# Optimization experiments

Measured on AMD Instinct MI355X. Metric: run time of the kernel, lower is better.

The kernel has to match this reference:

```python
import jax, jax.numpy as jnp
import numpy as np

N_HEAD = 16
MASKED_BIAS = -10000.0


def setup_inputs() -> dict:
    key = jax.random.key(0)
    k1, k2, k3 = jax.random.split(key, 3)
    B, T, E = 2, 2048, 1024
    return {
        "stacked": jax.random.normal(k1, (B, T, E), dtype=jnp.float32),
        "w_attn": jax.random.normal(k2, (E, 3 * E), dtype=jnp.float32) * 0.02,
        "b_attn": jnp.zeros((3 * E,), dtype=jnp.float32),
        "w_proj": jax.random.normal(k3, (E, E), dtype=jnp.float32) * 0.02,
        "b_proj": jnp.zeros((E,), dtype=jnp.float32),
    }


def reference(stacked, w_attn, b_attn, w_proj, b_proj):
    B, T, E = stacked.shape
    nh = N_HEAD
    dh = E // nh
    # Conv1D (GPT-2): x @ W + b
    qkv = stacked @ w_attn + b_attn            # (B, T, 3E)
    q, k, v = jnp.split(qkv, 3, axis=-1)
    q = q.reshape(B, T, nh, dh).transpose(0, 2, 1, 3)  # (B, nh, T, dh)
    k = k.reshape(B, T, nh, dh).transpose(0, 2, 1, 3)
    v = v.reshape(B, T, nh, dh).transpose(0, 2, 1, 3)
    # scores = Q @ K^T / sqrt(dh)
    w = jnp.einsum("bhtd,bhsd->bhts", q, k) / jnp.sqrt(jnp.float32(dh))
    causal = jnp.tril(jnp.ones((T, T), dtype=bool))
    w = jnp.where(causal, w, jnp.float32(MASKED_BIAS))
    w = jax.nn.softmax(w, axis=-1)
    out = jnp.einsum("bhts,bhsd->bhtd", w, v)  # (B, nh, T, dh)
    out = out.transpose(0, 2, 1, 3).reshape(B, T, E)
    attn_z = out @ w_proj + b_proj
    return attn_z
```

## Files before the change

kernel.cpp:

```cpp
#include <hip/hip_runtime.h>
#include <hip/hip_bf16.h>

#define B_ 2
#define T_ 2048
#define E_ 1024
#define NH 16
#define M_ (B_*T_)
#define N3E 3072

typedef __attribute__((ext_vector_type(8))) short short8;
typedef __attribute__((ext_vector_type(4))) float f32x4;

__device__ __forceinline__ unsigned short f2bf(float f) {
  unsigned u = __builtin_bit_cast(unsigned, f);
  unsigned r = 0x7FFFu + ((u >> 16) & 1u);
  return (unsigned short)((u + r) >> 16);
}

__device__ __forceinline__ float bf2f(unsigned short s) {
  return __builtin_bit_cast(float, ((unsigned)s) << 16);
}

__device__ __forceinline__ unsigned cvtpk(float a, float b) {
  unsigned r;
  asm("v_cvt_pk_bf16_f32 %0, %1, %2" : "=v"(r) : "v"(a), "v"(b));
  return r;
}

__device__ __forceinline__ float exp2fast(float x) {
  float r;
  asm("v_exp_f32 %0, %1" : "=v"(r) : "v"(x));
  return r;
}

__device__ __forceinline__ void gload16(const void* g, void* l) {
  __builtin_amdgcn_global_load_lds(
      (const __attribute__((address_space(1))) unsigned int*)g,
      (__attribute__((address_space(3))) unsigned int*)l, 16, 0, 0);
}

__device__ __forceinline__ f32x4 mfma16(short8 a, short8 b, f32x4 c) {
  return __builtin_amdgcn_mfma_f32_16x16x32_bf16(a, b, c, 0, 0, 0);
}

__global__ __launch_bounds__(256) void prep_kernel(
    const float* __restrict__ stacked, const float* __restrict__ w_attn,
    const float* __restrict__ w_proj, unsigned short* __restrict__ Abf,
    unsigned short* __restrict__ WaT, unsigned short* __restrict__ WpT) {
  __shared__ float tile[32][33];
  const int bx = blockIdx.x;
  const int tid = threadIdx.x;
  if (bx < 2048) {
    int i = bx * 256 + tid;
    const float4* p = (const float4*)stacked + (size_t)i * 2;
    float4 a = p[0], b = p[1];
    short8 o;
    o[0] = (short)f2bf(a.x); o[1] = (short)f2bf(a.y);
    o[2] = (short)f2bf(a.z); o[3] = (short)f2bf(a.w);
    o[4] = (short)f2bf(b.x); o[5] = (short)f2bf(b.y);
    o[6] = (short)f2bf(b.z); o[7] = (short)f2bf(b.w);
    *(short8*)(Abf + (size_t)i * 8) = o;
    return;
  }
  const float* in;
  unsigned short* out;
  int R, C, c0, r0;
  if (bx < 5120) {
    int b = bx - 2048;
    in = w_attn; out = WaT; R = E_; C = N3E;
    c0 = (b % 96) * 32; r0 = (b / 96) * 32;
  } else {
    int b = bx - 5120;
    in = w_proj; out = WpT; R = E_; C = E_;
    c0 = (b % 32) * 32; r0 = (b / 32) * 32;
  }
  int tx = tid & 31, ty = tid >> 5;
#pragma unroll
  for (int i = 0; i < 4; i++) {
    int r = ty + i * 8;
    tile[r][tx] = in[(size_t)(r0 + r) * C + c0 + tx];
  }
  __syncthreads();
#pragma unroll
  for (int i = 0; i < 4; i++) {
    int r = ty + i * 8;
    out[(size_t)(c0 + r) * R + r0 + tx] = f2bf(tile[tx][r]);
  }
}

__global__ __launch_bounds__(512, 1) void gemm256(
    const unsigned short* __restrict__ A, const unsigned short* __restrict__ Bt,
    const float* __restrict__ bias, unsigned short* __restrict__ qkvout,
    unsigned short* __restrict__ Vt, int M, int N, int K) {
  __shared__ __attribute__((aligned(16))) unsigned short Asm[2][256 * 64];
  __shared__ __attribute__((aligned(16))) unsigned short Bsm[2][192 * 64];
  const int tid = threadIdx.x;
  const int lane = tid & 63, wid = tid >> 6;
  const int wr = wid >> 2, wcn = wid & 3;
  const int li = lane & 15, g = lane >> 4;
  const int sw = li & 7;

  const int ntx = N / 192;
  const int nwg = (M >> 8) * ntx;
  const int cpx = nwg >> 3;
  const int logical = (blockIdx.x & 7) * cpx + (blockIdx.x >> 3);
  const int bm = (logical / ntx) << 8;
  const int bn = (logical % ntx) * 192;

  f32x4 acc[8][3] = {};

#pragma unroll
  for (int p = 0; p < 4; p++) {
    int idx = tid + p * 512;
    int r = idx >> 3, ch = idx & 7;
    gload16(A + (size_t)(bm + r) * K + ((ch ^ (r & 7)) << 3),
            (char*)&Asm[0][0] + idx * 16);
  }
#pragma unroll
  for (int p = 0; p < 3; p++) {
    int idx = tid + p * 512;
    int r = idx >> 3, ch = idx & 7;
    gload16(Bt + (size_t)(bn + r) * K + ((ch ^ (r & 7)) << 3),
            (char*)&Bsm[0][0] + idx * 16);
  }
  asm volatile("s_waitcnt vmcnt(0)" ::: "memory");
  __syncthreads();

  const int NT = K >> 6;
  for (int t = 0; t < NT; t++) {
    const int buf = t & 1;
    const unsigned short* As = &Asm[buf][0];
    const unsigned short* Bs = &Bsm[buf][0];
    const int kn = (t + 1) << 6;
    const bool pre = (t + 1 < NT);
    short8 a[4][2];
#pragma unroll
    for (int ph = 0; ph < 6; ph++) {
      const int mh = ph / 3, nf3 = ph % 3;
      if (nf3 == 0) {
#pragma unroll
        for (int mf = 0; mf < 4; mf++) {
          const int R = wr * 128 + (mh * 4 + mf) * 16 + li;
          a[mf][0] = *(const short8*)&As[R * 64 + ((g ^ sw) << 3)];
          a[mf][1] = *(const short8*)&As[R * 64 + (((4 + g) ^ sw) << 3)];
        }
      }
      const int S = wcn * 48 + nf3 * 16 + li;
      short8 b0 = *(const short8*)&Bs[S * 64 + ((g ^ sw) << 3)];
      short8 b1 = *(const short8*)&Bs[S * 64 + (((4 + g) ^ sw) << 3)];
      if (pre && ph == 0) {
#pragma unroll
        for (int p = 0; p < 4; p++) {
          int idx = tid + p * 512;
          int r = idx >> 3, ch = idx & 7;
          gload16(A + (size_t)(bm + r) * K + kn + ((ch ^ (r & 7)) << 3),
                  (char*)&Asm[buf ^ 1][0] + idx * 16);
        }
      }
      if (pre && ph == 1) {
#pragma unroll
        for (int p = 0; p < 3; p++) {
          int idx = tid + p * 512;
          int r = idx >> 3, ch = idx & 7;
          gload16(Bt + (size_t)(bn + r) * K + kn + ((ch ^ (r & 7)) << 3),
                  (char*)&Bsm[buf ^ 1][0] + idx * 16);
        }
      }
      __builtin_amdgcn_sched_barrier(0);
      __builtin_amdgcn_s_setprio(1);
#pragma unroll
      for (int mf = 0; mf < 4; mf++) {
        f32x4 c = acc[mh * 4 + mf][nf3];
        c = mfma16(a[mf][0], b0, c);
        c = mfma16(a[mf][1], b1, c);
        acc[mh * 4 + mf][nf3] = c;
      }
      __builtin_amdgcn_s_setprio(0);
      __builtin_amdgcn_sched_barrier(0);
    }
    asm volatile("s_waitcnt vmcnt(0)" ::: "memory");
    __syncthreads();
  }

#pragma unroll
  for (int nf = 0; nf < 3; nf++) {
    int col = bn + wcn * 48 + nf * 16 + li;
    float bs = bias[col];
    if (col < 2 * E_) {
#pragma unroll
      for (int mf = 0; mf < 8; mf++) {
        int row0 = bm + wr * 128 + mf * 16 + g * 4;
#pragma unroll
        for (int r = 0; r < 4; r++)
          qkvout[(size_t)(row0 + r) * N + col] = f2bf(acc[mf][nf][r] + bs);
      }
    } else {
      const int c = col - 2 * E_;
#pragma unroll
      for (int mf = 0; mf < 8; mf++) {
        int row0 = bm + wr * 128 + mf * 16 + g * 4;
        int bq = row0 >> 11, s0 = row0 & 2047;
        uint2 o;
        o.x = cvtpk(acc[mf][nf][0] + bs, acc[mf][nf][1] + bs);
        o.y = cvtpk(acc[mf][nf][2] + bs, acc[mf][nf][3] + bs);
        *(uint2*)&Vt[(size_t)(bq * E_ + c) * T_ + s0] = o;
      }
    }
  }
}

template <int OUTF32>
__global__ __launch_bounds__(256) void gemm_bt(
    const unsigned short* __restrict__ A, const unsigned short* __restrict__ Bt,
    const float* __restrict__ bias, void* __restrict__ outp,
    int M, int N, int K) {
  __shared__ __attribute__((aligned(16))) unsigned short Asm[2][128 * 32];
  __shared__ __attribute__((aligned(16))) unsigned short Bsm[2][128 * 32];
  const int tid = threadIdx.x;
  const int lane = tid & 63;
  const int wid = tid >> 6;
  const int wr = wid >> 1, wc = wid & 1;
  const int li = lane & 15, g = lane >> 4;

  const int ntx = N >> 7;
  const int nwg = (M >> 7) * ntx;
  const int cpx = nwg >> 3;
  const int logical = (blockIdx.x & 7) * cpx + (blockIdx.x >> 3);
  const int bm = (logical / ntx) << 7;
  const int bn = (logical % ntx) << 7;

  f32x4 acc[4][4] = {};

  const int srow = tid >> 2;
  const int scol = (tid & 3) * 8;
  const unsigned short* Ag = A + (size_t)(bm + srow) * K + scol;
  const unsigned short* Bg = Bt + (size_t)(bn + srow) * K + scol;
  const int ldsoff = tid * 16;

  gload16(Ag, (char*)&Asm[0][0] + ldsoff);
  gload16(Ag + (size_t)64 * K, (char*)&Asm[0][0] + ldsoff + 4096);
  gload16(Bg, (char*)&Bsm[0][0] + ldsoff);
  gload16(Bg + (size_t)64 * K, (char*)&Bsm[0][0] + ldsoff + 4096);
  asm volatile("s_waitcnt vmcnt(0)" ::: "memory");
  __syncthreads();

  int cur = 0;
  for (int k0 = 0; k0 < K; k0 += 32) {
    const bool pre = (k0 + 32 < K);
    if (pre) {
      const int k1 = k0 + 32;
      gload16(Ag + k1, (char*)&Asm[cur ^ 1][0] + ldsoff);
      gload16(Ag + (size_t)64 * K + k1,
              (char*)&Asm[cur ^ 1][0] + ldsoff + 4096);
      gload16(Bg + k1, (char*)&Bsm[cur ^ 1][0] + ldsoff);
      gload16(Bg + (size_t)64 * K + k1,
              (char*)&Bsm[cur ^ 1][0] + ldsoff + 4096);
    }
    short8 af[4], bf[4];
#pragma unroll
    for (int i = 0; i < 4; i++)
      af[i] = *(const short8*)&Asm[cur][(wr * 64 + i * 16 + li) * 32 + g * 8];
#pragma unroll
    for (int j = 0; j < 4; j++)
      bf[j] = *(const short8*)&Bsm[cur][(wc * 64 + j * 16 + li) * 32 + g * 8];
    __builtin_amdgcn_s_setprio(1);
#pragma unroll
    for (int i = 0; i < 4; i++)
#pragma unroll
      for (int j = 0; j < 4; j++)
        acc[i][j] = __builtin_amdgcn_mfma_f32_16x16x32_bf16(af[i], bf[j],
                                                            acc[i][j], 0, 0, 0);
    __builtin_amdgcn_s_setprio(0);
    if (pre) asm volatile("s_waitcnt vmcnt(0)" ::: "memory");
    __syncthreads();
    cur ^= 1;
  }

#pragma unroll
  for (int j = 0; j < 4; j++) {
    int col = bn + wc * 64 + j * 16 + li;
    float bs = bias[col];
#pragma unroll
    for (int i = 0; i < 4; i++) {
      int row0 = bm + wr * 64 + i * 16 + g * 4;
#pragma unroll
      for (int r = 0; r < 4; r++) {
        float v = acc[i][j][r] + bs;
        if (OUTF32)
          ((float*)outp)[(size_t)(row0 + r) * N + col] = v;
        else
          ((unsigned short*)outp)[(size_t)(row0 + r) * N + col] = f2bf(v);
      }
    }
  }
}

__device__ __forceinline__ void attn_tile(
    const unsigned short* Ksm, const unsigned short* Vts,
    unsigned short (*PsmW)[64], short8 qf0, short8 qf1,
    float& m2, float& l2, f32x4* O, int qrel, bool diag, int li, int g) {
  f32x4 S[4];
  __builtin_amdgcn_s_setprio(1);
#pragma unroll
  for (int ct = 0; ct < 4; ct++) {
    int r = ct * 16 + li;
    int sw = r & 7;
    short8 k0f = *(const short8*)&Ksm[r * 64 + ((g ^ sw) << 3)];
    short8 k1f = *(const short8*)&Ksm[r * 64 + (((g + 4) ^ sw) << 3)];
    f32x4 z = {0.f, 0.f, 0.f, 0.f};
    z = mfma16(k0f, qf0, z);
    z = mfma16(k1f, qf1, z);
    S[ct] = z;
  }
  __builtin_amdgcn_s_setprio(0);

  if (diag) {
#pragma unroll
    for (int ct = 0; ct < 4; ct++)
#pragma unroll
      for (int r = 0; r < 4; r++)
        if (ct * 16 + g * 4 + r > qrel) S[ct][r] = -30000.f;
  }

  float tmax = S[0][0];
#pragma unroll
  for (int ct = 0; ct < 4; ct++)
#pragma unroll
    for (int r = 0; r < 4; r++) tmax = fmaxf(tmax, S[ct][r]);
  tmax = fmaxf(tmax, __shfl_xor(tmax, 16));
  tmax = fmaxf(tmax, __shfl_xor(tmax, 32));

  if (__any(tmax > m2 + 11.5f)) {
    float mn = fmaxf(m2, tmax);
    float cs = exp2fast(m2 - mn);
    l2 *= cs;
#pragma unroll
    for (int c2 = 0; c2 < 4; c2++)
#pragma unroll
      for (int r = 0; r < 4; r++) O[c2][r] *= cs;
    m2 = mn;
  }

  float rsum = 0.f;
#pragma unroll
  for (int ct = 0; ct < 4; ct++) {
    float p0 = exp2fast(S[ct][0] - m2);
    float p1 = exp2fast(S[ct][1] - m2);
    float p2 = exp2fast(S[ct][2] - m2);
    float p3 = exp2fast(S[ct][3] - m2);
    rsum += (p0 + p1) + (p2 + p3);
    uint2 pk;
    pk.x = cvtpk(p0, p1);
    pk.y = cvtpk(p2, p3);
    int pc = (2 * ct + (g >> 1)) ^ (li & 7);
    *(uint2*)&PsmW[li][pc * 8 + (g & 1) * 4] = pk;
  }
  rsum += __shfl_xor(rsum, 16);
  rsum += __shfl_xor(rsum, 32);
  l2 += rsum;

  __builtin_amdgcn_s_setprio(1);
#pragma unroll
  for (int kk = 0; kk < 2; kk++) {
    short8 pf = *(const short8*)&PsmW[li][((4 * kk + g) ^ (li & 7)) * 8];
#pragma unroll
    for (int c2 = 0; c2 < 4; c2++) {
      int d = c2 * 16 + li;
      short8 vf = *(const short8*)&Vts[d * 64 + (((kk * 4 + g) ^ (li & 7)) << 3)];
      O[c2] = mfma16(vf, pf, O[c2]);
    }
  }
  __builtin_amdgcn_s_setprio(0);
}

__global__ __launch_bounds__(256) void attn_kernel(
    const unsigned short* __restrict__ qkv, const unsigned short* __restrict__ Vt,
    unsigned short* __restrict__ aout) {
  const int pair = blockIdx.x;
  const int h = blockIdx.y, b = blockIdx.z;
  const int qa = pair, qb = (T_ / 64 - 1) - pair;
  const int tid = threadIdx.x, lane = tid & 63, w = tid >> 6;
  const int li = lane & 15, g = lane >> 4;

  __shared__ __attribute__((aligned(16))) unsigned short Ksm[2][64 * 64];
  __shared__ __attribute__((aligned(16))) unsigned short Vts[2][64 * 64];
  __shared__ __attribute__((aligned(16))) unsigned short Psm[4][16][64];

  const size_t rs = 3 * E_;
  const unsigned short* base = qkv + (size_t)b * T_ * rs + h * 64;
  const unsigned short* Kg = base + E_;
  const unsigned short* Vtg = Vt + (size_t)(b * E_ + h * 64) * T_;

  const float QSC = 0.18033688f;
  short8 qfa0, qfa1, qfb0, qfb1;
  {
    const unsigned short* qrow = base + (size_t)(qa * 64 + w * 16 + li) * rs;
    short8 v0 = *(const short8*)(qrow + g * 8);
    short8 v1 = *(const short8*)(qrow + 32 + g * 8);
    qrow = base + (size_t)(qb * 64 + w * 16 + li) * rs;
    short8 v2 = *(const short8*)(qrow + g * 8);
    short8 v3 = *(const short8*)(qrow + 32 + g * 8);
#pragma unroll
    for (int j = 0; j < 8; j++) {
      qfa0[j] = (short)f2bf(bf2f((unsigned short)v0[j]) * QSC);
      qfa1[j] = (short)f2bf(bf2f((unsigned short)v1[j]) * QSC);
      qfb0[j] = (short)f2bf(bf2f((unsigned short)v2[j]) * QSC);
      qfb1[j] = (short)f2bf(bf2f((unsigned short)v3[j]) * QSC);
    }
  }

  float ma = -1e30f, la = 0.f, mb = -1e30f, lb = 0.f;
  f32x4 Oa[4] = {}, Ob[4] = {};

#pragma unroll
  for (int p = 0; p < 2; p++) {
    int idx = tid + p * 256;
    int r = idx >> 3, ch = idx & 7;
    int sc = (ch ^ (r & 7)) * 8;
    gload16(Kg + (size_t)r * rs + sc, (char*)&Ksm[0][0] + idx * 16);
    gload16(Vtg + (size_t)r * T_ + sc, (char*)&Vts[0][0] + idx * 16);
  }
  asm volatile("s_waitcnt vmcnt(0)" ::: "memory");
  __syncthreads();

  const int nt = qb + 1;
  for (int kv = 0; kv < nt; kv++) {
    const int cur = kv & 1, nxt = cur ^ 1;
    const bool pre = (kv + 1 < nt);
    if (pre) {
      const int s1 = (kv + 1) * 64;
#pragma unroll
      for (int p = 0; p < 2; p++) {
        int idx = tid + p * 256;
        int r = idx >> 3, ch = idx & 7;
        int sc = (ch ^ (r & 7)) * 8;
        gload16(Kg + (size_t)(s1 + r) * rs + sc,
                (char*)&Ksm[nxt][0] + idx * 16);
        gload16(Vtg + (size_t)r * T_ + s1 + sc,
                (char*)&Vts[nxt][0] + idx * 16);
      }
    }

    attn_tile(&Ksm[cur][0], &Vts[cur][0], Psm[w], qfb0, qfb1, mb, lb, Ob,
              qb * 64 + w * 16 + li - kv * 64, kv == qb, li, g);
    if (kv <= qa)
      attn_tile(&Ksm[cur][0], &Vts[cur][0], Psm[w], qfa0, qfa1, ma, la, Oa,
                qa * 64 + w * 16 + li - kv * 64, kv == qa, li, g);

    asm volatile("s_waitcnt vmcnt(0)" ::: "memory");
    __syncthreads();
  }

  const float inva = 1.f / la, invb = 1.f / lb;
  const int rowa = b * T_ + qa * 64 + w * 16 + li;
  const int rowb = b * T_ + qb * 64 + w * 16 + li;
#pragma unroll
  for (int c2 = 0; c2 < 4; c2++) {
    uint2 oa, ob;
    oa.x = cvtpk(Oa[c2][0] * inva, Oa[c2][1] * inva);
    oa.y = cvtpk(Oa[c2][2] * inva, Oa[c2][3] * inva);
    ob.x = cvtpk(Ob[c2][0] * invb, Ob[c2][1] * invb);
    ob.y = cvtpk(Ob[c2][2] * invb, Ob[c2][3] * invb);
    *(uint2*)&aout[(size_t)rowa * E_ + h * 64 + c2 * 16 + g * 4] = oa;
    *(uint2*)&aout[(size_t)rowb * E_ + h * 64 + c2 * 16 + g * 4] = ob;
  }
}

extern "C" void kernel_launch(void* const* d_in, const int* in_sizes, int n_in,
                              void* d_out, int out_size, void* d_ws,
                              size_t ws_size, hipStream_t stream) {
  const float* stacked = (const float*)d_in[0];
  const float* w_attn = (const float*)d_in[1];
  const float* b_attn = (const float*)d_in[2];
  const float* w_proj = (const float*)d_in[3];
  const float* b_proj = (const float*)d_in[4];
  float* out = (float*)d_out;

  unsigned short* Abf = (unsigned short*)d_ws;
  unsigned short* WaT = Abf + (size_t)M_ * E_;
  unsigned short* WpT = WaT + (size_t)N3E * E_;
  unsigned short* qkv = WpT + (size_t)E_ * E_;
  unsigned short* aout = qkv + (size_t)M_ * N3E;
  unsigned short* Vt = aout + (size_t)M_ * E_;

  prep_kernel<<<6144, 256, 0, stream>>>(stacked, w_attn, w_proj, Abf, WaT, WpT);
  gemm256<<<(M_ / 256) * (N3E / 192), 512, 0, stream>>>(Abf, WaT, b_attn, qkv,
                                                        Vt, M_, N3E, E_);
  attn_kernel<<<dim3(T_ / 128, NH, B_), 256, 0, stream>>>(qkv, Vt, aout);
  gemm_bt<1><<<(M_ / 128) * (E_ / 128), 256, 0, stream>>>(aout, WpT, b_proj,
                                                          out, M_, E_, E_);
}
```

Measured before the change: 114.5 us.

## Stage 128-key KV tiles in attention and hoist GEMM prefetch to loop top

```diff
diff --git a/kernel.cpp b/kernel.cpp
--- a/kernel.cpp
+++ b/kernel.cpp
@@ -133,6 +133,22 @@
     const unsigned short* Bs = &Bsm[buf][0];
     const int kn = (t + 1) << 6;
     const bool pre = (t + 1 < NT);
+    if (pre) {
+#pragma unroll
+      for (int p = 0; p < 4; p++) {
+        int idx = tid + p * 512;
+        int r = idx >> 3, ch = idx & 7;
+        gload16(A + (size_t)(bm + r) * K + kn + ((ch ^ (r & 7)) << 3),
+                (char*)&Asm[buf ^ 1][0] + idx * 16);
+      }
+#pragma unroll
+      for (int p = 0; p < 3; p++) {
+        int idx = tid + p * 512;
+        int r = idx >> 3, ch = idx & 7;
+        gload16(Bt + (size_t)(bn + r) * K + kn + ((ch ^ (r & 7)) << 3),
+                (char*)&Bsm[buf ^ 1][0] + idx * 16);
+      }
+    }
     short8 a[4][2];
 #pragma unroll
     for (int ph = 0; ph < 6; ph++) {
@@ -148,24 +164,6 @@
       const int S = wcn * 48 + nf3 * 16 + li;
       short8 b0 = *(const short8*)&Bs[S * 64 + ((g ^ sw) << 3)];
       short8 b1 = *(const short8*)&Bs[S * 64 + (((4 + g) ^ sw) << 3)];
-      if (pre && ph == 0) {
-#pragma unroll
-        for (int p = 0; p < 4; p++) {
-          int idx = tid + p * 512;
-          int r = idx >> 3, ch = idx & 7;
-          gload16(A + (size_t)(bm + r) * K + kn + ((ch ^ (r & 7)) << 3),
-                  (char*)&Asm[buf ^ 1][0] + idx * 16);
-        }
-      }
-      if (pre && ph == 1) {
-#pragma unroll
-        for (int p = 0; p < 3; p++) {
-          int idx = tid + p * 512;
-          int r = idx >> 3, ch = idx & 7;
-          gload16(Bt + (size_t)(bn + r) * K + kn + ((ch ^ (r & 7)) << 3),
-                  (char*)&Bsm[buf ^ 1][0] + idx * 16);
-        }
-      }
       __builtin_amdgcn_sched_barrier(0);
       __builtin_amdgcn_s_setprio(1);
 #pragma unroll
@@ -300,11 +298,11 @@
     unsigned short (*PsmW)[64], short8 qf0, short8 qf1,
     float& m2, float& l2, f32x4* O, int qrel, bool diag, int li, int g) {
   f32x4 S[4];
+  const int sw = li & 7;
   __builtin_amdgcn_s_setprio(1);
 #pragma unroll
   for (int ct = 0; ct < 4; ct++) {
     int r = ct * 16 + li;
-    int sw = r & 7;
     short8 k0f = *(const short8*)&Ksm[r * 64 + ((g ^ sw) << 3)];
     short8 k1f = *(const short8*)&Ksm[r * 64 + (((g + 4) ^ sw) << 3)];
     f32x4 z = {0.f, 0.f, 0.f, 0.f};
@@ -352,7 +350,7 @@
     uint2 pk;
     pk.x = cvtpk(p0, p1);
     pk.y = cvtpk(p2, p3);
-    int pc = (2 * ct + (g >> 1)) ^ (li & 7);
+    int pc = (2 * ct + (g >> 1)) ^ sw;
     *(uint2*)&PsmW[li][pc * 8 + (g & 1) * 4] = pk;
   }
   rsum += __shfl_xor(rsum, 16);
@@ -362,11 +360,11 @@
   __builtin_amdgcn_s_setprio(1);
 #pragma unroll
   for (int kk = 0; kk < 2; kk++) {
-    short8 pf = *(const short8*)&PsmW[li][((4 * kk + g) ^ (li & 7)) * 8];
+    short8 pf = *(const short8*)&PsmW[li][((4 * kk + g) ^ sw) * 8];
 #pragma unroll
     for (int c2 = 0; c2 < 4; c2++) {
       int d = c2 * 16 + li;
-      short8 vf = *(const short8*)&Vts[d * 64 + (((kk * 4 + g) ^ (li & 7)) << 3)];
+      short8 vf = *(const short8*)&Vts[d * 128 + (((kk * 4 + g) ^ sw) << 3)];
       O[c2] = mfma16(vf, pf, O[c2]);
     }
   }
@@ -382,8 +380,8 @@
   const int tid = threadIdx.x, lane = tid & 63, w = tid >> 6;
   const int li = lane & 15, g = lane >> 4;
 
-  __shared__ __attribute__((aligned(16))) unsigned short Ksm[2][64 * 64];
-  __shared__ __attribute__((aligned(16))) unsigned short Vts[2][64 * 64];
+  __shared__ __attribute__((aligned(16))) unsigned short Ksm[2][128 * 64];
+  __shared__ __attribute__((aligned(16))) unsigned short Vts[2][64 * 128];
   __shared__ __attribute__((aligned(16))) unsigned short Psm[4][16][64];
 
   const size_t rs = 3 * E_;
@@ -412,48 +410,60 @@
   float ma = -1e30f, la = 0.f, mb = -1e30f, lb = 0.f;
   f32x4 Oa[4] = {}, Ob[4] = {};
 
-#pragma unroll
-  for (int p = 0; p < 2; p++) {
-    int idx = tid + p * 256;
-    int r = idx >> 3, ch = idx & 7;
-    int sc = (ch ^ (r & 7)) * 8;
-    gload16(Kg + (size_t)r * rs + sc, (char*)&Ksm[0][0] + idx * 16);
-    gload16(Vtg + (size_t)r * T_ + sc, (char*)&Vts[0][0] + idx * 16);
-  }
+  const int qrow_b = qb * 64 + w * 16 + li;
+  const int qrow_a = qa * 64 + w * 16 + li;
+
+#define STAGE_TILE(kv, bf)                                                    \
+  {                                                                           \
+    _Pragma("unroll") for (int p = 0; p < 4; p++) {                           \
+      int idx = tid + p * 256;                                                \
+      int r = idx >> 3, ch = idx & 7;                                         \
+      int sc = (ch ^ (r & 7)) * 8;                                            \
+      gload16(Kg + (size_t)((kv)*128 + r) * rs + sc,                          \
+              (char*)&Ksm[bf][0] + idx * 16);                                 \
+    }                                                                         \
+    _Pragma("unroll") for (int p = 0; p < 4; p++) {                           \
+      int idx = tid + p * 256;                                                \
+      int d = idx >> 4, c = idx & 15;                                         \
+      int sc = ((c & 8) | ((c & 7) ^ (d & 7))) * 8;                           \
+      gload16(Vtg + (size_t)d * T_ + (kv)*128 + sc,                           \
+              (char*)&Vts[bf][0] + idx * 16);                                 \
+    }                                                                         \
+  }
+
+  STAGE_TILE(0, 0);
   asm volatile("s_waitcnt vmcnt(0)" ::: "memory");
   __syncthreads();
 
-  const int nt = qb + 1;
-  for (int kv = 0; kv < nt; kv++) {
+  const int ntb = qb / 2 + 1;
+  const int nta = qa / 2 + 1;
+  for (int kv = 0; kv < ntb; kv++) {
     const int cur = kv & 1, nxt = cur ^ 1;
-    const bool pre = (kv + 1 < nt);
-    if (pre) {
-      const int s1 = (kv + 1) * 64;
-#pragma unroll
-      for (int p = 0; p < 2; p++) {
-        int idx = tid + p * 256;
-        int r = idx >> 3, ch = idx & 7;
-        int sc = (ch ^ (r & 7)) * 8;
-        gload16(Kg + (size_t)(s1 + r) * rs + sc,
-                (char*)&Ksm[nxt][0] + idx * 16);
-        gload16(Vtg + (size_t)r * T_ + s1 + sc,
-                (char*)&Vts[nxt][0] + idx * 16);
-      }
-    }
-
+    const bool pre = (kv + 1 < ntb);
+    if (pre) STAGE_TILE(kv + 1, nxt);
+
+    const int s64 = kv * 2;
     attn_tile(&Ksm[cur][0], &Vts[cur][0], Psm[w], qfb0, qfb1, mb, lb, Ob,
-              qb * 64 + w * 16 + li - kv * 64, kv == qb, li, g);
-    if (kv <= qa)
+              qrow_b - s64 * 64, s64 == qb, li, g);
+    if (s64 + 1 <= qb)
+      attn_tile(&Ksm[cur][4096], &Vts[cur][64], Psm[w], qfb0, qfb1, mb, lb,
+                Ob, qrow_b - (s64 + 1) * 64, s64 + 1 == qb, li, g);
+    if (kv < nta) {
       attn_tile(&Ksm[cur][0], &Vts[cur][0], Psm[w], qfa0, qfa1, ma, la, Oa,
-                qa * 64 + w * 16 + li - kv * 64, kv == qa, li, g);
+                qrow_a - s64 * 64, s64 == qa, li, g);
+      if (s64 + 1 <= qa)
+        attn_tile(&Ksm[cur][4096], &Vts[cur][64], Psm[w], qfa0, qfa1, ma, la,
+                  Oa, qrow_a - (s64 + 1) * 64, s64 + 1 == qa, li, g);
+    }
 
     asm volatile("s_waitcnt vmcnt(0)" ::: "memory");
     __syncthreads();
   }
+#undef STAGE_TILE
 
   const float inva = 1.f / la, invb = 1.f / lb;
-  const int rowa = b * T_ + qa * 64 + w * 16 + li;
-  const int rowb = b * T_ + qb * 64 + w * 16 + li;
+  const int rowa = b * T_ + qrow_a;
+  const int rowb = b * T_ + qrow_b;
 #pragma unroll
   for (int c2 = 0; c2 < 4; c2++) {
     uint2 oa, ob;
```

Result: no change. 114.9 us (+0.4%).

## Restructure double-buffered prefetch to use partial vmcnt waits across three kernels

Applied to the files above, without the earlier changes.

```diff
diff --git a/kernel.cpp b/kernel.cpp
--- a/kernel.cpp
+++ b/kernel.cpp
@@ -109,30 +109,36 @@
 
   f32x4 acc[8][3] = {};
 
-#pragma unroll
-  for (int p = 0; p < 4; p++) {
-    int idx = tid + p * 512;
-    int r = idx >> 3, ch = idx & 7;
-    gload16(A + (size_t)(bm + r) * K + ((ch ^ (r & 7)) << 3),
-            (char*)&Asm[0][0] + idx * 16);
-  }
-#pragma unroll
-  for (int p = 0; p < 3; p++) {
-    int idx = tid + p * 512;
-    int r = idx >> 3, ch = idx & 7;
-    gload16(Bt + (size_t)(bn + r) * K + ((ch ^ (r & 7)) << 3),
-            (char*)&Bsm[0][0] + idx * 16);
-  }
-  asm volatile("s_waitcnt vmcnt(0)" ::: "memory");
-  __syncthreads();
+#define G256_STAGE(kk0, bf)                                                   \
+  {                                                                           \
+    _Pragma("unroll") for (int p = 0; p < 4; p++) {                           \
+      int idx = tid + p * 512;                                                \
+      int r = idx >> 3, ch = idx & 7;                                         \
+      gload16(A + (size_t)(bm + r) * K + (kk0) + ((ch ^ (r & 7)) << 3),       \
+              (char*)&Asm[bf][0] + idx * 16);                                 \
+    }                                                                         \
+    _Pragma("unroll") for (int p = 0; p < 3; p++) {                           \
+      int idx = tid + p * 512;                                                \
+      int r = idx >> 3, ch = idx & 7;                                         \
+      gload16(Bt + (size_t)(bn + r) * K + (kk0) + ((ch ^ (r & 7)) << 3),      \
+              (char*)&Bsm[bf][0] + idx * 16);                                 \
+    }                                                                         \
+  }
+
+  G256_STAGE(0, 0);
 
   const int NT = K >> 6;
   for (int t = 0; t < NT; t++) {
     const int buf = t & 1;
     const unsigned short* As = &Asm[buf][0];
     const unsigned short* Bs = &Bsm[buf][0];
-    const int kn = (t + 1) << 6;
     const bool pre = (t + 1 < NT);
+    if (pre) G256_STAGE((t + 1) << 6, buf ^ 1);
+    if (pre)
+      asm volatile("s_waitcnt vmcnt(7)" ::: "memory");
+    else
+      asm volatile("s_waitcnt vmcnt(0)" ::: "memory");
+    __syncthreads();
     short8 a[4][2];
 #pragma unroll
     for (int ph = 0; ph < 6; ph++) {
@@ -148,24 +154,6 @@
       const int S = wcn * 48 + nf3 * 16 + li;
       short8 b0 = *(const short8*)&Bs[S * 64 + ((g ^ sw) << 3)];
       short8 b1 = *(const short8*)&Bs[S * 64 + (((4 + g) ^ sw) << 3)];
-      if (pre && ph == 0) {
-#pragma unroll
-        for (int p = 0; p < 4; p++) {
-          int idx = tid + p * 512;
-          int r = idx >> 3, ch = idx & 7;
-          gload16(A + (size_t)(bm + r) * K + kn + ((ch ^ (r & 7)) << 3),
-                  (char*)&Asm[buf ^ 1][0] + idx * 16);
-        }
-      }
-      if (pre && ph == 1) {
-#pragma unroll
-        for (int p = 0; p < 3; p++) {
-          int idx = tid + p * 512;
-          int r = idx >> 3, ch = idx & 7;
-          gload16(Bt + (size_t)(bn + r) * K + kn + ((ch ^ (r & 7)) << 3),
-                  (char*)&Bsm[buf ^ 1][0] + idx * 16);
-        }
-      }
       __builtin_amdgcn_sched_barrier(0);
       __builtin_amdgcn_s_setprio(1);
 #pragma unroll
@@ -178,9 +166,9 @@
       __builtin_amdgcn_s_setprio(0);
       __builtin_amdgcn_sched_barrier(0);
     }
-    asm volatile("s_waitcnt vmcnt(0)" ::: "memory");
-    __syncthreads();
-  }
+    __syncthreads();
+  }
+#undef G256_STAGE
 
 #pragma unroll
   for (int nf = 0; nf < 3; nf++) {
@@ -237,25 +225,25 @@
   const unsigned short* Bg = Bt + (size_t)(bn + srow) * K + scol;
   const int ldsoff = tid * 16;
 
-  gload16(Ag, (char*)&Asm[0][0] + ldsoff);
-  gload16(Ag + (size_t)64 * K, (char*)&Asm[0][0] + ldsoff + 4096);
-  gload16(Bg, (char*)&Bsm[0][0] + ldsoff);
-  gload16(Bg + (size_t)64 * K, (char*)&Bsm[0][0] + ldsoff + 4096);
-  asm volatile("s_waitcnt vmcnt(0)" ::: "memory");
-  __syncthreads();
+#define GBT_STAGE(kk0, bf)                                                    \
+  {                                                                           \
+    gload16(Ag + (kk0), (char*)&Asm[bf][0] + ldsoff);                         \
+    gload16(Ag + (size_t)64 * K + (kk0), (char*)&Asm[bf][0] + ldsoff + 4096); \
+    gload16(Bg + (kk0), (char*)&Bsm[bf][0] + ldsoff);                         \
+    gload16(Bg + (size_t)64 * K + (kk0), (char*)&Bsm[bf][0] + ldsoff + 4096); \
+  }
+
+  GBT_STAGE(0, 0);
 
   int cur = 0;
   for (int k0 = 0; k0 < K; k0 += 32) {
     const bool pre = (k0 + 32 < K);
-    if (pre) {
-      const int k1 = k0 + 32;
-      gload16(Ag + k1, (char*)&Asm[cur ^ 1][0] + ldsoff);
-      gload16(Ag + (size_t)64 * K + k1,
-              (char*)&Asm[cur ^ 1][0] + ldsoff + 4096);
-      gload16(Bg + k1, (char*)&Bsm[cur ^ 1][0] + ldsoff);
-      gload16(Bg + (size_t)64 * K + k1,
-              (char*)&Bsm[cur ^ 1][0] + ldsoff + 4096);
-    }
+    if (pre) GBT_STAGE(k0 + 32, cur ^ 1);
+    if (pre)
+      asm volatile("s_waitcnt vmcnt(4)" ::: "memory");
+    else
+      asm volatile("s_waitcnt vmcnt(0)" ::: "memory");
+    __syncthreads();
     short8 af[4], bf[4];
 #pragma unroll
     for (int i = 0; i < 4; i++)
@@ -271,10 +259,10 @@
         acc[i][j] = __builtin_amdgcn_mfma_f32_16x16x32_bf16(af[i], bf[j],
                                                             acc[i][j], 0, 0, 0);
     __builtin_amdgcn_s_setprio(0);
-    if (pre) asm volatile("s_waitcnt vmcnt(0)" ::: "memory");
     __syncthreads();
     cur ^= 1;
   }
+#undef GBT_STAGE
 
 #pragma unroll
   for (int j = 0; j < 4; j++) {
@@ -412,34 +400,31 @@
   float ma = -1e30f, la = 0.f, mb = -1e30f, lb = 0.f;
   f32x4 Oa[4] = {}, Ob[4] = {};
 
-#pragma unroll
-  for (int p = 0; p < 2; p++) {
-    int idx = tid + p * 256;
-    int r = idx >> 3, ch = idx & 7;
-    int sc = (ch ^ (r & 7)) * 8;
-    gload16(Kg + (size_t)r * rs + sc, (char*)&Ksm[0][0] + idx * 16);
-    gload16(Vtg + (size_t)r * T_ + sc, (char*)&Vts[0][0] + idx * 16);
-  }
-  asm volatile("s_waitcnt vmcnt(0)" ::: "memory");
-  __syncthreads();
+#define ATT_STAGE(kv, bf)                                                     \
+  {                                                                           \
+    _Pragma("unroll") for (int p = 0; p < 2; p++) {                           \
+      int idx = tid + p * 256;                                                \
+      int r = idx >> 3, ch = idx & 7;                                         \
+      int sc = (ch ^ (r & 7)) * 8;                                            \
+      gload16(Kg + (size_t)((kv)*64 + r) * rs + sc,                           \
+              (char*)&Ksm[bf][0] + idx * 16);                                 \
+      gload16(Vtg + (size_t)r * T_ + (kv)*64 + sc,                            \
+              (char*)&Vts[bf][0] + idx * 16);                                 \
+    }                                                                         \
+  }
+
+  ATT_STAGE(0, 0);
 
   const int nt = qb + 1;
   for (int kv = 0; kv < nt; kv++) {
     const int cur = kv & 1, nxt = cur ^ 1;
     const bool pre = (kv + 1 < nt);
-    if (pre) {
-      const int s1 = (kv + 1) * 64;
-#pragma unroll
-      for (int p = 0; p < 2; p++) {
-        int idx = tid + p * 256;
-        int r = idx >> 3, ch = idx & 7;
-        int sc = (ch ^ (r & 7)) * 8;
-        gload16(Kg + (size_t)(s1 + r) * rs + sc,
-                (char*)&Ksm[nxt][0] + idx * 16);
-        gload16(Vtg + (size_t)r * T_ + s1 + sc,
-                (char*)&Vts[nxt][0] + idx * 16);
-      }
-    }
+    if (pre) ATT_STAGE(kv + 1, nxt);
+    if (pre)
+      asm volatile("s_waitcnt vmcnt(4)" ::: "memory");
+    else
+      asm volatile("s_waitcnt vmcnt(0)" ::: "memory");
+    __syncthreads();
 
     attn_tile(&Ksm[cur][0], &Vts[cur][0], Psm[w], qfb0, qfb1, mb, lb, Ob,
               qb * 64 + w * 16 + li - kv * 64, kv == qb, li, g);
@@ -447,9 +432,9 @@
       attn_tile(&Ksm[cur][0], &Vts[cur][0], Psm[w], qfa0, qfa1, ma, la, Oa,
                 qa * 64 + w * 16 + li - kv * 64, kv == qa, li, g);
 
-    asm volatile("s_waitcnt vmcnt(0)" ::: "memory");
-    __syncthreads();
-  }
+    __syncthreads();
+  }
+#undef ATT_STAGE
 
   const float inva = 1.f / la, invb = 1.f / lb;
   const int rowa = b * T_ + qa * 64 + w * 16 + li;
```

Result: slower. 129.3 us (+12.9%).
